# Kernel optimization log

Measured on AMD Instinct MI355X. Metric: run time of the kernel, lower is better.

## Reference

```python
import jax, jax.numpy as jnp
import numpy as np

D_MODEL = 768
NHEAD = 12
HEAD_DIM = D_MODEL // NHEAD
WINDOW = 33  # band half-width = 16


def setup_inputs() -> dict:
    key = jax.random.key(0)
    ks = jax.random.split(key, 9)
    B, T, C = 2, 4096, D_MODEL
    s = 0.02
    return {
        "x": jax.random.normal(ks[0], (B, T, C), jnp.float32),
        "Wq": jax.random.normal(ks[1], (C, C), jnp.float32) * s,
        "bq": jnp.zeros((C,), jnp.float32),
        "Wk": jax.random.normal(ks[2], (C, C), jnp.float32) * s,
        "bk": jnp.zeros((C,), jnp.float32),
        "Wv": jax.random.normal(ks[3], (C, C), jnp.float32) * s,
        "bv": jnp.zeros((C,), jnp.float32),
        "Wo": jax.random.normal(ks[4], (C, C), jnp.float32) * s,
        "bo": jnp.zeros((C,), jnp.float32),
    }


def reference(x, Wq, bq, Wk, bk, Wv, bv, Wo, bo):
    B, T, C = x.shape
    H, D = NHEAD, HEAD_DIM
    scale = D ** -0.5
    # torch Linear: x @ W.T + b
    q = (x @ Wq.T + bq).reshape(B, T, H, D).transpose(0, 2, 1, 3)  # [B,H,T,D]
    k = (x @ Wk.T + bk).reshape(B, T, H, D).transpose(0, 2, 1, 3)
    v = (x @ Wv.T + bv).reshape(B, T, H, D).transpose(0, 2, 1, 3)
    scores = jnp.einsum("bhqd,bhkd->bhqk", q, k) * scale  # [B,H,T,T]
    idx = jnp.arange(T)
    local_mask = jnp.abs(idx[:, None] - idx[None, :]) <= (WINDOW // 2)  # [T,T]
    scores = jnp.where(local_mask[None, None], scores, -jnp.inf)
    attn = jax.nn.softmax(scores, axis=-1)  # dropout=0 / eval mode
    out = jnp.einsum("bhqk,bhkd->bhqd", attn, v)  # [B,H,T,D]
    out = out.transpose(0, 2, 1, 3).reshape(B, T, C)
    return out @ Wo.T + bo
```

## Files before the change

kernel.cpp:

```cpp
#include <hip/hip_runtime.h>
#include <math.h>
#include <cstdint>
#include <cstddef>

typedef unsigned short u16;
typedef short bf16x8 __attribute__((ext_vector_type(8)));
typedef float f32x4 __attribute__((ext_vector_type(4)));
typedef u16 u16x8 __attribute__((ext_vector_type(8)));
typedef u16 u16x4 __attribute__((ext_vector_type(4)));

#define T_LEN 4096
#define NH 12
#define HD 64
#define DMODEL 768
#define GK 768
#define QKV_STRIDE 6291456ul

__device__ __forceinline__ u16 f2bf(float x) {
  union { float f; unsigned u; } v; v.f = x;
  unsigned r = v.u + 0x7fffu + ((v.u >> 16) & 1u);
  return (u16)(r >> 16);
}

__device__ __forceinline__ void async16(const u16* g, u16* l) {
  __builtin_amdgcn_global_load_lds(
      (const __attribute__((address_space(1))) unsigned int*)g,
      (__attribute__((address_space(3))) unsigned int*)l, 16, 0, 0);
}

__global__ void cvt_all(const float* __restrict__ x,
                        const float* __restrict__ Wq, const float* __restrict__ Wk,
                        const float* __restrict__ Wv, const float* __restrict__ Wo,
                        u16* __restrict__ xb, u16* __restrict__ wqkv, u16* __restrict__ wo_b) {
  int bx = blockIdx.x;
  const float* s; u16* d; int base;
  if (bx < 6144)      { s = x;  d = xb;             base = bx; }
  else if (bx < 6720) { s = Wq; d = wqkv;           base = bx - 6144; }
  else if (bx < 7296) { s = Wk; d = wqkv + 589824;  base = bx - 6720; }
  else if (bx < 7872) { s = Wv; d = wqkv + 1179648; base = bx - 7296; }
  else                { s = Wo; d = wo_b;           base = bx - 7872; }
  int i = (base * 256 + (int)threadIdx.x) * 4;
  float4 v = *(const float4*)(s + i);
  u16x4 o;
  o[0] = f2bf(v.x); o[1] = f2bf(v.y); o[2] = f2bf(v.z); o[3] = f2bf(v.w);
  *(u16x4*)(d + i) = o;
}

#define BN 128
#define BK 32

template <int EPI, int MI>
__global__ __launch_bounds__(256)
void gemm_bt(const u16* __restrict__ A, const u16* __restrict__ B,
             const float* __restrict__ bias0, const float* __restrict__ bias1,
             void* __restrict__ outp) {
  constexpr int BMt = MI * 32;
  __shared__ __align__(16) u16 As[BMt * BK];
  __shared__ __align__(16) u16 Bs[BN * BK];

  const int tid  = threadIdx.x;
  const int lane = tid & 63;
  const int wave = tid >> 6;
  const int wm = wave & 1, wn = wave >> 1;
  const long am0 = (long)blockIdx.x * BMt;
  const long bn0 = (long)blockIdx.y * BN;
  const int r16 = lane & 15;
  const int kh  = lane >> 4;
  const int sw8 = (kh ^ ((r16 >> 1) & 3)) * 8;

  f32x4 acc[MI][4] = {};

  const int srow   = lane >> 2;
  const int schunk = ((lane & 3) ^ ((lane >> 3) & 3)) * 8;
  const u16* Ag = A + (am0 + wave * 16 + srow) * GK + schunk;
  const u16* Bg = B + (bn0 + wave * 16 + srow) * GK + schunk;
  u16* Bl0 = &Bs[(wave * 16) * BK];
  u16* Bl1 = &Bs[(64 + wave * 16) * BK];

  for (int kt = 0; kt < GK; kt += BK) {
    __syncthreads();
#pragma unroll
    for (int s = 0; s < MI / 2; s++)
      async16(Ag + (size_t)(s * 64) * GK + kt, &As[(s * 64 + wave * 16) * BK]);
    async16(Bg + kt, Bl0);
    async16(Bg + 64 * GK + kt, Bl1);
    __syncthreads();
    bf16x8 af[MI], bfr[4];
#pragma unroll
    for (int i = 0; i < MI; i++)
      af[i] = *(const bf16x8*)&As[(wm * MI * 16 + i * 16 + r16) * BK + sw8];
#pragma unroll
    for (int j = 0; j < 4; j++)
      bfr[j] = *(const bf16x8*)&Bs[(wn * 64 + j * 16 + r16) * BK + sw8];
#pragma unroll
    for (int i = 0; i < MI; i++)
#pragma unroll
      for (int j = 0; j < 4; j++)
        acc[i][j] = __builtin_amdgcn_mfma_f32_16x16x32_bf16(af[i], bfr[j], acc[i][j], 0, 0, 0);
  }

  const int m0 = (int)am0 + wm * MI * 16;

  if (EPI == 0) {
    const int tens = (int)(bn0 >= 768);
    const int c0 = (int)bn0 - tens * 768;
    const float* bp = tens ? bias1 : bias0;
    u16* outb = (u16*)outp + (size_t)tens * QKV_STRIDE;
#pragma unroll
    for (int j = 0; j < 4; j++) {
      int col = c0 + wn * 64 + j * 16 + r16;
      float bv = bp[col];
#pragma unroll
      for (int i = 0; i < MI; i++) {
#pragma unroll
        for (int r = 0; r < 4; r++) {
          int row = m0 + i * 16 + kh * 4 + r;
          outb[(size_t)row * DMODEL + col] = f2bf(acc[i][j][r] + bv);
        }
      }
    }
  } else if (EPI == 2) {
    u16* vtb = (u16*)outp;
    const int kr = kh * 4;
#pragma unroll
    for (int j = 0; j < 4; j++) {
      int cl = (int)bn0 + wn * 64 + j * 16;
      int hj = cl >> 6;
      int dlane = (cl & 63) + r16;
      float bv = bias0[cl + r16];
#pragma unroll
      for (int i = 0; i < MI; i++) {
        int row0 = m0 + i * 16;
        int b_ = row0 >> 12;
        int tb = (row0 & 4095) >> 4;
        size_t base = (((size_t)(b_ * NH + hj) * 256 + tb) << 10) + dlane * 16 + kr;
        u16x4 pk;
#pragma unroll
        for (int r = 0; r < 4; r++) pk[r] = f2bf(acc[i][j][r] + bv);
        *(u16x4*)(vtb + base) = pk;
      }
    }
  } else {
    float* O = (float*)outp;
#pragma unroll
    for (int i = 0; i < MI; i++) {
#pragma unroll
      for (int r = 0; r < 4; r++) {
        int row = m0 + i * 16 + kh * 4 + r;
        float* orow = O + (size_t)row * DMODEL;
#pragma unroll
        for (int j = 0; j < 4; j++) {
          int col = (int)bn0 + wn * 64 + j * 16 + r16;
          orow[col] = acc[i][j][r] + bias0[col];
        }
      }
    }
  }
}

#define PSS 72

__global__ __launch_bounds__(256)
void attn_mfma(const u16* __restrict__ qkv, const u16* __restrict__ vt,
               u16* __restrict__ attn) {
  __shared__ __align__(16) u16 Ps[4][16 * PSS];
  const int tid = threadIdx.x, lane = tid & 63, wave = tid >> 6;
  const int r16 = lane & 15, quad = lane >> 4;
  const int q0 = blockIdx.x * 64;
  const int h = blockIdx.y, b = blockIdx.z;
  const long rowbase = (long)b * T_LEN;
  const int hc = h * HD;
  const u16* Qg = qkv;
  const u16* Kg = qkv + QKV_STRIDE;
  const u16* Vh = vt + ((size_t)(b * NH + h)) * (256 * 1024);

  const int qbase = q0 + wave * 16;
  const int kb = qbase - 16;

  const u16* qrow = Qg + (rowbase + qbase + r16) * DMODEL + hc + quad * 8;
  bf16x8 qa0 = *(const bf16x8*)qrow;
  bf16x8 qa1 = *(const bf16x8*)(qrow + 32);

  f32x4 s[3];
#pragma unroll
  for (int t = 0; t < 3; t++) {
    const u16* krow = Kg + (rowbase + kb + t * 16 + r16) * DMODEL + hc + quad * 8;
    bf16x8 kf0 = *(const bf16x8*)krow;
    bf16x8 kf1 = *(const bf16x8*)(krow + 32);
    f32x4 a = {};
    a = __builtin_amdgcn_mfma_f32_16x16x32_bf16(qa0, kf0, a, 0, 0, 0);
    a = __builtin_amdgcn_mfma_f32_16x16x32_bf16(qa1, kf1, a, 0, 0, 0);
    s[t] = a;
  }

  float pr[3][4];
#pragma unroll
  for (int r = 0; r < 4; r++) {
    const int qg = qbase + quad * 4 + r;
    float sc[3];
#pragma unroll
    for (int t = 0; t < 3; t++) {
      int key = kb + t * 16 + r16;
      bool ok = (key >= qg - 16) && (key <= qg + 16) && (key >= 0) && (key < T_LEN);
      sc[t] = ok ? s[t][r] * 0.125f : -INFINITY;
    }
    float mx = fmaxf(sc[0], fmaxf(sc[1], sc[2]));
    mx = fmaxf(mx, __shfl_xor(mx, 1));
    mx = fmaxf(mx, __shfl_xor(mx, 2));
    mx = fmaxf(mx, __shfl_xor(mx, 4));
    mx = fmaxf(mx, __shfl_xor(mx, 8));
    float e0 = __expf(sc[0] - mx), e1 = __expf(sc[1] - mx), e2 = __expf(sc[2] - mx);
    float l = e0 + e1 + e2;
    l += __shfl_xor(l, 1);
    l += __shfl_xor(l, 2);
    l += __shfl_xor(l, 4);
    l += __shfl_xor(l, 8);
    float inv = 1.0f / l;
    pr[0][r] = e0 * inv; pr[1][r] = e1 * inv; pr[2][r] = e2 * inv;
  }

  u16* psw = &Ps[wave][0];
#pragma unroll
  for (int t = 0; t < 3; t++)
#pragma unroll
    for (int r = 0; r < 4; r++)
      psw[(quad * 4 + r) * PSS + t * 16 + r16] = f2bf(pr[t][r]);
#pragma unroll
  for (int r = 0; r < 4; r++)
    psw[(quad * 4 + r) * PSS + 48 + r16] = 0;

  bf16x8 pa0 = *(const bf16x8*)&psw[r16 * PSS + quad * 8];
  bf16x8 pa1 = *(const bf16x8*)&psw[r16 * PSS + 32 + quad * 8];

  const int kq1 = kb + quad * 8;
  const int kq2 = kb + 32 + quad * 8;
  const int o1 = (kq1 >> 4) * 1024 + (kq1 & 15);
  const int o2 = (kq2 >> 4) * 1024 + (kq2 & 15);
  f32x4 o[4];
#pragma unroll
  for (int c = 0; c < 4; c++) {
    const u16* vb = Vh + (16 * c + r16) * 16;
    bf16x8 v1 = *(const bf16x8*)(vb + o1);
    bf16x8 v2 = *(const bf16x8*)(vb + o2);
    f32x4 a = {};
    a = __builtin_amdgcn_mfma_f32_16x16x32_bf16(pa0, v1, a, 0, 0, 0);
    a = __builtin_amdgcn_mfma_f32_16x16x32_bf16(pa1, v2, a, 0, 0, 0);
    o[c] = a;
  }

#pragma unroll
  for (int c = 0; c < 4; c++) {
#pragma unroll
    for (int r = 0; r < 4; r++) {
      int qg = qbase + quad * 4 + r;
      attn[(rowbase + qg) * DMODEL + hc + 16 * c + r16] = f2bf(o[c][r]);
    }
  }
}

extern "C" void kernel_launch(void* const* d_in, const int* in_sizes, int n_in,
                              void* d_out, int out_size, void* d_ws, size_t ws_size,
                              hipStream_t stream) {
  const float* x  = (const float*)d_in[0];
  const float* Wq = (const float*)d_in[1];
  const float* bq = (const float*)d_in[2];
  const float* Wk = (const float*)d_in[3];
  const float* bk = (const float*)d_in[4];
  const float* Wv = (const float*)d_in[5];
  const float* bv = (const float*)d_in[6];
  const float* Wo = (const float*)d_in[7];
  const float* bo = (const float*)d_in[8];
  float* out = (float*)d_out;
  char* ws = (char*)d_ws;

  u16* xb   = (u16*)(ws);
  u16* wqkv = (u16*)(ws + 12582912);
  u16* wo_b = (u16*)(ws + 16121856);
  u16* qkv  = (u16*)(ws + 17301504);
  u16* attnb = (u16*)(ws + 55050240);

  cvt_all<<<8448, 256, 0, stream>>>(x, Wq, Wk, Wv, Wo, xb, wqkv, wo_b);

  gemm_bt<0, 4><<<dim3(64, 12), 256, 0, stream>>>(xb, wqkv, bq, bk, (void*)qkv);
  gemm_bt<2, 4><<<dim3(64, 6), 256, 0, stream>>>(xb, wqkv + 1179648, bv, bv,
                                                 (void*)(qkv + 2 * QKV_STRIDE));
  attn_mfma<<<dim3(64, 12, 2), 256, 0, stream>>>(qkv, qkv + 2 * QKV_STRIDE, attnb);
  gemm_bt<1, 2><<<dim3(128, 6), 256, 0, stream>>>(attnb, wo_b, bo, bo, (void*)out);
}
```

Baseline: 171.3 us.

## Register-prefetch GEMM tiles and stage attention output through LDS for wide stores

The GEMM main loop stops using direct global-to-LDS async loads with a sync before each tile. It now prefetches the next K tile into registers while the current tile is computed, then writes it into swizzled LDS. This is meant to overlap global memory latency with MFMA work, at the cost of more registers and two barriers per iteration. The attention epilogue also writes its output through an LDS scratch buffer (psw), so each lane can issue 16-byte coalesced stores instead of scattered 2-byte stores.

```diff
diff --git a/kernel.cpp b/kernel.cpp
--- a/kernel.cpp
+++ b/kernel.cpp
@@ -20,12 +20,6 @@
   union { float f; unsigned u; } v; v.f = x;
   unsigned r = v.u + 0x7fffu + ((v.u >> 16) & 1u);
   return (u16)(r >> 16);
-}
-
-__device__ __forceinline__ void async16(const u16* g, u16* l) {
-  __builtin_amdgcn_global_load_lds(
-      (const __attribute__((address_space(1))) unsigned int*)g,
-      (__attribute__((address_space(3))) unsigned int*)l, 16, 0, 0);
 }
 
 __global__ void cvt_all(const float* __restrict__ x,
@@ -55,6 +49,7 @@
              const float* __restrict__ bias0, const float* __restrict__ bias1,
              void* __restrict__ outp) {
   constexpr int BMt = MI * 32;
+  constexpr int NK = GK / BK;
   __shared__ __align__(16) u16 As[BMt * BK];
   __shared__ __align__(16) u16 Bs[BN * BK];
 
@@ -70,21 +65,32 @@
 
   f32x4 acc[MI][4] = {};
 
-  const int srow   = lane >> 2;
-  const int schunk = ((lane & 3) ^ ((lane >> 3) & 3)) * 8;
-  const u16* Ag = A + (am0 + wave * 16 + srow) * GK + schunk;
-  const u16* Bg = B + (bn0 + wave * 16 + srow) * GK + schunk;
-  u16* Bl0 = &Bs[(wave * 16) * BK];
-  u16* Bl1 = &Bs[(64 + wave * 16) * BK];
-
-  for (int kt = 0; kt < GK; kt += BK) {
-    __syncthreads();
-#pragma unroll
-    for (int s = 0; s < MI / 2; s++)
-      async16(Ag + (size_t)(s * 64) * GK + kt, &As[(s * 64 + wave * 16) * BK]);
-    async16(Bg + kt, Bl0);
-    async16(Bg + 64 * GK + kt, Bl1);
-    __syncthreads();
+  const int rb = tid >> 1;
+  const int gb = (tid & 1) * 2;
+  const int sb = (rb >> 1) & 3;
+  const u16* Bgp = B + (bn0 + rb) * GK + gb * 8;
+  u16* Bw0 = &Bs[rb * BK + ((gb)     ^ sb) * 8];
+  u16* Bw1 = &Bs[rb * BK + ((gb + 1) ^ sb) * 8];
+  const int ra = (MI == 4) ? (tid >> 1) : (tid >> 2);
+  const int ga = (MI == 4) ? ((tid & 1) * 2) : (tid & 3);
+  const int sa = (ra >> 1) & 3;
+  const u16* Agp = A + (am0 + ra) * GK + ga * 8;
+  u16* Aw0 = &As[ra * BK + ((ga)     ^ sa) * 8];
+  u16* Aw1 = &As[ra * BK + (((ga + 1) & 3) ^ sa) * 8];
+
+  uint4 rA0, rA1, rB0, rB1;
+  auto loadT = [&](int kt) {
+    rB0 = *(const uint4*)(Bgp + kt);
+    rB1 = *(const uint4*)(Bgp + kt + 8);
+    rA0 = *(const uint4*)(Agp + kt);
+    if (MI == 4) rA1 = *(const uint4*)(Agp + kt + 8);
+  };
+  auto writeT = [&]() {
+    *(uint4*)Bw0 = rB0; *(uint4*)Bw1 = rB1;
+    *(uint4*)Aw0 = rA0;
+    if (MI == 4) *(uint4*)Aw1 = rA1;
+  };
+  auto mfma_tile = [&]() {
     bf16x8 af[MI], bfr[4];
 #pragma unroll
     for (int i = 0; i < MI; i++)
@@ -97,6 +103,20 @@
 #pragma unroll
       for (int j = 0; j < 4; j++)
         acc[i][j] = __builtin_amdgcn_mfma_f32_16x16x32_bf16(af[i], bfr[j], acc[i][j], 0, 0, 0);
+  };
+
+  loadT(0);
+  writeT();
+  loadT(BK);
+  __syncthreads();
+  for (int k = 0; k < NK; k++) {
+    mfma_tile();
+    if (k + 1 < NK) {
+      __syncthreads();
+      writeT();
+      if (k + 2 < NK) loadT((k + 2) * BK);
+      __syncthreads();
+    }
   }
 
   const int m0 = (int)am0 + wm * MI * 16;
@@ -249,12 +269,17 @@
   }
 
 #pragma unroll
-  for (int c = 0; c < 4; c++) {
-#pragma unroll
-    for (int r = 0; r < 4; r++) {
-      int qg = qbase + quad * 4 + r;
-      attn[(rowbase + qg) * DMODEL + hc + 16 * c + r16] = f2bf(o[c][r]);
-    }
+  for (int c = 0; c < 4; c++)
+#pragma unroll
+    for (int r = 0; r < 4; r++)
+      psw[(quad * 4 + r) * PSS + 16 * c + r16] = f2bf(o[c][r]);
+  {
+    int rr = lane >> 3, cc = (lane & 7) * 8;
+    u16x8 v0 = *(const u16x8*)&psw[rr * PSS + cc];
+    u16x8 v1 = *(const u16x8*)&psw[(8 + rr) * PSS + cc];
+    u16* ob = attn + (rowbase + qbase) * DMODEL + hc;
+    *(u16x8*)(ob + (size_t)rr * DMODEL + cc) = v0;
+    *(u16x8*)(ob + (size_t)(8 + rr) * DMODEL + cc) = v1;
   }
 }
 
```

New measurement: 172.5 us. About the same (+0.7%).

## Remap GEMM blocks per XCD and coalesce attention output stores via LDS

Applied to the files above, without the earlier changes.

GEMM kernels now take a flattened 1D grid and remap block ids so consecutive row tiles land on the same XCD, aiming for better L2 reuse of operand tiles. The attention kernel stages its bf16 output tile in shared memory and writes it with 16-byte vector stores instead of scattered 2-byte stores. This adds an LDS round-trip and relies on an existing per-wave shared buffer.

```diff
diff --git a/kernel.cpp b/kernel.cpp
--- a/kernel.cpp
+++ b/kernel.cpp
@@ -49,21 +49,28 @@
 #define BN 128
 #define BK 32
 
-template <int EPI, int MI>
+template <int EPI, int MI, int NX>
 __global__ __launch_bounds__(256)
 void gemm_bt(const u16* __restrict__ A, const u16* __restrict__ B,
              const float* __restrict__ bias0, const float* __restrict__ bias1,
              void* __restrict__ outp) {
   constexpr int BMt = MI * 32;
+  constexpr int PER = NX / 8;
   __shared__ __align__(16) u16 As[BMt * BK];
   __shared__ __align__(16) u16 Bs[BN * BK];
+
+  const int bid  = blockIdx.x;
+  const int xcd  = bid & 7;
+  const int slot = bid >> 3;
+  const int bx   = xcd * PER + (slot % PER);
+  const int by   = slot / PER;
 
   const int tid  = threadIdx.x;
   const int lane = tid & 63;
   const int wave = tid >> 6;
   const int wm = wave & 1, wn = wave >> 1;
-  const long am0 = (long)blockIdx.x * BMt;
-  const long bn0 = (long)blockIdx.y * BN;
+  const long am0 = (long)bx * BMt;
+  const long bn0 = (long)by * BN;
   const int r16 = lane & 15;
   const int kh  = lane >> 4;
   const int sw8 = (kh ^ ((r16 >> 1) & 3)) * 8;
@@ -249,12 +256,17 @@
   }
 
 #pragma unroll
-  for (int c = 0; c < 4; c++) {
-#pragma unroll
-    for (int r = 0; r < 4; r++) {
-      int qg = qbase + quad * 4 + r;
-      attn[(rowbase + qg) * DMODEL + hc + 16 * c + r16] = f2bf(o[c][r]);
-    }
+  for (int c = 0; c < 4; c++)
+#pragma unroll
+    for (int r = 0; r < 4; r++)
+      psw[(quad * 4 + r) * PSS + 16 * c + r16] = f2bf(o[c][r]);
+  {
+    int rr = lane >> 3, cc = (lane & 7) * 8;
+    u16x8 v0 = *(const u16x8*)&psw[rr * PSS + cc];
+    u16x8 v1 = *(const u16x8*)&psw[(8 + rr) * PSS + cc];
+    u16* ob = attn + (rowbase + qbase) * DMODEL + hc;
+    *(u16x8*)(ob + (size_t)rr * DMODEL + cc) = v0;
+    *(u16x8*)(ob + (size_t)(8 + rr) * DMODEL + cc) = v1;
   }
 }
 
@@ -281,9 +293,9 @@
 
   cvt_all<<<8448, 256, 0, stream>>>(x, Wq, Wk, Wv, Wo, xb, wqkv, wo_b);
 
-  gemm_bt<0, 4><<<dim3(64, 12), 256, 0, stream>>>(xb, wqkv, bq, bk, (void*)qkv);
-  gemm_bt<2, 4><<<dim3(64, 6), 256, 0, stream>>>(xb, wqkv + 1179648, bv, bv,
-                                                 (void*)(qkv + 2 * QKV_STRIDE));
+  gemm_bt<0, 4, 64><<<768, 256, 0, stream>>>(xb, wqkv, bq, bk, (void*)qkv);
+  gemm_bt<2, 4, 64><<<384, 256, 0, stream>>>(xb, wqkv + 1179648, bv, bv,
+                                             (void*)(qkv + 2 * QKV_STRIDE));
   attn_mfma<<<dim3(64, 12, 2), 256, 0, stream>>>(qkv, qkv + 2 * QKV_STRIDE, attnb);
-  gemm_bt<1, 2><<<dim3(128, 6), 256, 0, stream>>>(attnb, wo_b, bo, bo, (void*)out);
-}
+  gemm_bt<1, 2, 128><<<768, 256, 0, stream>>>(attnb, wo_b, bo, bo, (void*)out);
+}
```

Result: no change. 168.5 us (-1.6%).
